# Kernel tuning notes

Measured on AMD Instinct MI355X. Metric: run time of the kernel, lower is better.

Reference implementation:

```python
import jax, jax.numpy as jnp
import numpy as np

D = 3  # input dim, hardcoded in source


def _jet_linear(c0, c1, c2, W, b):
    # Taylor-mode (raw-derivative coefficients) through y = x @ W^T + b.
    # Bias only affects the 0th coefficient; higher coefficients are linear.
    y0 = jnp.einsum('bdi,oi->bdo', c0, W) + b
    y1 = jnp.einsum('bdi,oi->bdo', c1, W)
    y2 = jnp.einsum('bdi,oi->bdo', c2, W)
    return y0, y1, y2


def _jet_tanh(c0, c1, c2):
    # g(t) with g(0)=c0, g'(0)=c1, g''(0)=c2; f = tanh(g):
    #   f(0)  = tanh(c0)
    #   f'(0) = sech^2(c0) * c1
    #   f''(0)= sech^2(c0) * c2 - 2 tanh(c0) sech^2(c0) * c1^2
    y0 = jnp.tanh(c0)
    s = 1.0 - y0 * y0  # sech^2
    y1 = s * c1
    y2 = s * c2 - 2.0 * y0 * s * (c1 * c1)
    return y0, y1, y2


def setup_inputs() -> dict:
    key = jax.random.key(0)
    ks = jax.random.split(key, 7)
    B = 131072
    x = jax.random.normal(ks[0], (B, D), dtype=jnp.float32)
    # Kaiming-ish small init so tanh does not saturate
    W1 = jax.random.normal(ks[1], (128, D), dtype=jnp.float32) * (1.0 / np.sqrt(D))
    b1 = jax.random.normal(ks[2], (128,), dtype=jnp.float32) * 0.01
    W2 = jax.random.normal(ks[3], (64, 128), dtype=jnp.float32) * (1.0 / np.sqrt(128))
    b2 = jax.random.normal(ks[4], (64,), dtype=jnp.float32) * 0.01
    W3 = jax.random.normal(ks[5], (1, 64), dtype=jnp.float32) * (1.0 / np.sqrt(64))
    b3 = jax.random.normal(ks[6], (1,), dtype=jnp.float32) * 0.01
    return {'x': x, 'W1': W1, 'b1': b1, 'W2': W2, 'b2': b2, 'W3': W3, 'b3': b3}


def reference(x, W1, b1, W2, b2, W3, b3):
    # x: [B, D]. Propagate a k=2 jet along each of the D coordinate
    # directions (vmapped over the direction axis d), then sum the 2nd
    # coefficients -> Laplacian. Returns [B, 1].
    B = x.shape[0]
    dt = x.dtype
    X0 = jnp.broadcast_to(x[:, None, :], (B, D, D))            # replicate(x, D)
    X1 = jnp.broadcast_to(jnp.eye(D, dtype=dt), (B, D, D))     # eye(D)
    X2 = jnp.zeros((B, D, D), dtype=dt)                         # zeros(D, D)
    c = _jet_linear(X0, X1, X2, W1, b1)
    c = _jet_tanh(*c)
    c = _jet_linear(*c, W2, b2)
    c = _jet_tanh(*c)
    F0, F1, F2 = _jet_linear(*c, W3, b3)                        # F2: [B, D, 1]
    return F2.sum(axis=1)                                       # sum_vmapped -> [B, 1]
```

## Files before the change

### kernel.cpp

```cpp
#include <hip/hip_runtime.h>


typedef _Float16 h2 __attribute__((ext_vector_type(2)));
typedef _Float16 h4 __attribute__((ext_vector_type(4)));
typedef _Float16 h8 __attribute__((ext_vector_type(8)));
typedef float f32x4 __attribute__((ext_vector_type(4)));

#define BLOCK 256
constexpr int DH1 = 128;
constexpr int DH2 = 64;
constexpr int TILES = 2;

__device__ __forceinline__ float fast_tanh(float x) {
    float e = __builtin_amdgcn_exp2f(x * 2.885390081777926814f);
    return fmaf(-2.0f, __builtin_amdgcn_rcpf(e + 1.0f), 1.0f);
}

__device__ __forceinline__ h2 pk(float a, float b) {
    auto r = __builtin_amdgcn_cvt_pkrtz(a, b);
    return __builtin_bit_cast(h2, r);
}

__device__ __forceinline__ h8 cat4(h2 a, h2 b, h2 c, h2 d) {
    h4 lo = __builtin_shufflevector(a, b, 0, 1, 2, 3);
    h4 hi = __builtin_shufflevector(c, d, 0, 1, 2, 3);
    return __builtin_shufflevector(lo, hi, 0, 1, 2, 3, 4, 5, 6, 7);
}

__global__ __launch_bounds__(BLOCK) void lap_fused(
        const float* __restrict__ x,
        const float* __restrict__ W1, const float* __restrict__ b1,
        const float* __restrict__ W2, const float* __restrict__ b2,
        const float* __restrict__ W3,
        float* __restrict__ out, int B, int ntiles)
{
    __shared__ float4 s_w1p[DH1];
    __shared__ float  s_wq2[DH1];
    __shared__ __align__(16) _Float16 s_a[16][64][8];
    __shared__ __align__(16) float s_b2[DH2];
    __shared__ __align__(16) float s_w3[DH2];

    const int t = threadIdx.x;

    #pragma unroll
    for (int u = 0; u < 4; ++u) {
        const int f   = u * 256 + t;
        const int l   = f & 63;
        const int row = f >> 6;
        const int m   = row & 3;
        const int kk  = row >> 2;
        const int k   = m * 16 + (l & 15);
        const int jr  = kk * 32 + (l >> 4) * 8;
        const float4 wlo = *reinterpret_cast<const float4*>(W2 + k * DH1 + jr);
        const float4 whi = *reinterpret_cast<const float4*>(W2 + k * DH1 + jr + 4);
        *reinterpret_cast<h8*>(&s_a[row][l][0]) =
            cat4(pk(wlo.x, wlo.y), pk(wlo.z, wlo.w),
                 pk(whi.x, whi.y), pk(whi.z, whi.w));
    }
    if (t < DH1) {
        const float wx = W1[t*3+0], wy = W1[t*3+1], wz = W1[t*3+2];
        s_w1p[t] = make_float4(wx, wy, wz, b1[t]);
        s_wq2[t] = -2.0f * (wx*wx + wy*wy + wz*wz);
    }
    if (t < DH2) { s_b2[t] = b2[t]; s_w3[t] = W3[t]; }
    __syncthreads();

    const int lane = t & 63;
    const int wave = t >> 6;
    const int bcol = lane & 15;
    const int g    = lane >> 4;

    #pragma unroll 1
    for (int tile = 0; tile < TILES; ++tile) {
        const int tid = blockIdx.x + tile * gridDim.x;
        if (tid >= ntiles) break;
        const int braw = tid * 64 + wave * 16 + bcol;
        const int b    = (braw < B) ? braw : (B - 1);

        const float x0 = x[b*3+0];
        const float x1 = x[b*3+1];
        const float x2 = x[b*3+2];

        f32x4 acc[5][4];
        #pragma unroll
        for (int f = 0; f < 5; ++f)
            #pragma unroll
            for (int m = 0; m < 4; ++m)
                acc[f][m] = (f32x4){0.f, 0.f, 0.f, 0.f};

        #pragma unroll
        for (int kk = 0; kk < 4; ++kk) {
            h2 P0[4], P1[4], P2[4], P3[4], P4[4];
            #pragma unroll
            for (int ii = 0; ii < 4; ++ii) {
                const int j0 = kk*32 + g*8 + ii*2;
                const float4 wa = s_w1p[j0];
                const float4 wb = s_w1p[j0 + 1];
                const float  qa = s_wq2[j0];
                const float  qb = s_wq2[j0 + 1];

                const float prea = fmaf(x0, wa.x, fmaf(x1, wa.y, fmaf(x2, wa.z, wa.w)));
                const float ea   = __builtin_amdgcn_exp2f(prea * 2.885390081777926814f);
                const float ra   = __builtin_amdgcn_rcpf(ea + 1.0f);
                const float ha   = fmaf(-2.0f, ra, 1.0f);
                const float sa   = fmaf(-ha, ha, 1.0f);

                const float preb = fmaf(x0, wb.x, fmaf(x1, wb.y, fmaf(x2, wb.z, wb.w)));
                const float eb   = __builtin_amdgcn_exp2f(preb * 2.885390081777926814f);
                const float rb   = __builtin_amdgcn_rcpf(eb + 1.0f);
                const float hb   = fmaf(-2.0f, rb, 1.0f);
                const float sb   = fmaf(-hb, hb, 1.0f);

                P0[ii] = pk(ha,          hb);
                P1[ii] = pk(sa * wa.x,   sb * wb.x);
                P2[ii] = pk(sa * wa.y,   sb * wb.y);
                P3[ii] = pk(sa * wa.z,   sb * wb.z);
                P4[ii] = pk((ha*sa)*qa,  (hb*sb)*qb);
            }
            const h8 F0 = cat4(P0[0], P0[1], P0[2], P0[3]);
            const h8 F1 = cat4(P1[0], P1[1], P1[2], P1[3]);
            const h8 F2 = cat4(P2[0], P2[1], P2[2], P2[3]);
            const h8 F3 = cat4(P3[0], P3[1], P3[2], P3[3]);
            const h8 F4 = cat4(P4[0], P4[1], P4[2], P4[3]);

            #pragma unroll
            for (int m = 0; m < 4; ++m) {
                const h8 fa = *reinterpret_cast<const h8*>(&s_a[kk*4 + m][lane][0]);
                acc[0][m] = __builtin_amdgcn_mfma_f32_16x16x32_f16(fa, F0, acc[0][m], 0, 0, 0);
                acc[1][m] = __builtin_amdgcn_mfma_f32_16x16x32_f16(fa, F1, acc[1][m], 0, 0, 0);
                acc[2][m] = __builtin_amdgcn_mfma_f32_16x16x32_f16(fa, F2, acc[2][m], 0, 0, 0);
                acc[3][m] = __builtin_amdgcn_mfma_f32_16x16x32_f16(fa, F3, acc[3][m], 0, 0, 0);
                acc[4][m] = __builtin_amdgcn_mfma_f32_16x16x32_f16(fa, F4, acc[4][m], 0, 0, 0);
            }
        }

        float partial = 0.0f;
        #pragma unroll
        for (int m = 0; m < 4; ++m) {
            const int kb = m*16 + g*4;
            const f32x4 b2v = *reinterpret_cast<const f32x4*>(&s_b2[kb]);
            const f32x4 w3v = *reinterpret_cast<const f32x4*>(&s_w3[kb]);
            #pragma unroll
            for (int r = 0; r < 4; ++r) {
                const float z0 = acc[0][m][r] + b2v[r];
                const float g0 = fast_tanh(z0);
                const float s2 = fmaf(-g0, g0, 1.0f);
                const float qd = acc[1][m][r]*acc[1][m][r]
                               + acc[2][m][r]*acc[2][m][r]
                               + acc[3][m][r]*acc[3][m][r];
                const float G2 = s2 * fmaf(-2.0f * g0, qd, acc[4][m][r]);
                partial = fmaf(w3v[r], G2, partial);
            }
        }

        partial += __shfl_xor(partial, 16);
        partial += __shfl_xor(partial, 32);

        if (g == 0 && braw < B) out[braw] = partial;
    }
}

extern "C" void kernel_launch(void* const* d_in, const int* in_sizes, int n_in,
                              void* d_out, int out_size, void* d_ws, size_t ws_size,
                              hipStream_t stream) {
    const float* x  = (const float*)d_in[0];
    const float* W1 = (const float*)d_in[1];
    const float* b1 = (const float*)d_in[2];
    const float* W2 = (const float*)d_in[3];
    const float* b2 = (const float*)d_in[4];
    const float* W3 = (const float*)d_in[5];
    float* out = (float*)d_out;

    const int B      = in_sizes[0] / 3;
    const int ntiles = (B + 63) / 64;
    const int grid   = (ntiles + TILES - 1) / TILES;
    lap_fused<<<grid, BLOCK, 0, stream>>>(x, W1, b1, W2, b2, W3, out, B, ntiles);
}
```

Before: 25.95 us.

## Double block size, prefetch x for both tiles, fold tanh scale into weights

Blocks grow to 512 threads covering 128 batch rows per tile, which halves the grid and spreads the per-block W2 fp16 staging over twice as many rows. The x values for both tiles are loaded before the shared-memory setup, so their global latency overlaps the weight staging. The 2/ln2 tanh scale is folded into b1, b2 and x, which removes a multiply per activation. The grid drops to 512 blocks, so occupancy and load balance across CUs shift, and the larger blocks need more registers.

```diff
diff --git a/kernel.cpp b/kernel.cpp
--- a/kernel.cpp
+++ b/kernel.cpp
@@ -6,15 +6,11 @@
 typedef _Float16 h8 __attribute__((ext_vector_type(8)));
 typedef float f32x4 __attribute__((ext_vector_type(4)));
 
-#define BLOCK 256
+#define BLOCK 512
 constexpr int DH1 = 128;
 constexpr int DH2 = 64;
 constexpr int TILES = 2;
-
-__device__ __forceinline__ float fast_tanh(float x) {
-    float e = __builtin_amdgcn_exp2f(x * 2.885390081777926814f);
-    return fmaf(-2.0f, __builtin_amdgcn_rcpf(e + 1.0f), 1.0f);
-}
+constexpr float CTANH = 2.885390081777926814f;
 
 __device__ __forceinline__ h2 pk(float a, float b) {
     auto r = __builtin_amdgcn_cvt_pkrtz(a, b);
@@ -37,14 +33,29 @@
     __shared__ float4 s_w1p[DH1];
     __shared__ float  s_wq2[DH1];
     __shared__ __align__(16) _Float16 s_a[16][64][8];
-    __shared__ __align__(16) float s_b2[DH2];
+    __shared__ __align__(16) float s_b2c[DH2];
     __shared__ __align__(16) float s_w3[DH2];
 
-    const int t = threadIdx.x;
+    const int t    = threadIdx.x;
+    const int lane = t & 63;
+    const int wave = t >> 6;
+    const int bcol = lane & 15;
+    const int g    = lane >> 4;
+
+    float xv[TILES][3];
+    #pragma unroll
+    for (int tile = 0; tile < TILES; ++tile) {
+        const int tid  = blockIdx.x + tile * gridDim.x;
+        const int braw = tid * 128 + wave * 16 + bcol;
+        const int b    = (braw < B) ? braw : (B - 1);
+        xv[tile][0] = x[b*3+0];
+        xv[tile][1] = x[b*3+1];
+        xv[tile][2] = x[b*3+2];
+    }
 
     #pragma unroll
-    for (int u = 0; u < 4; ++u) {
-        const int f   = u * 256 + t;
+    for (int u = 0; u < 2; ++u) {
+        const int f   = u * 512 + t;
         const int l   = f & 63;
         const int row = f >> 6;
         const int m   = row & 3;
@@ -59,27 +70,21 @@
     }
     if (t < DH1) {
         const float wx = W1[t*3+0], wy = W1[t*3+1], wz = W1[t*3+2];
-        s_w1p[t] = make_float4(wx, wy, wz, b1[t]);
+        s_w1p[t] = make_float4(wx, wy, wz, CTANH * b1[t]);
         s_wq2[t] = -2.0f * (wx*wx + wy*wy + wz*wz);
     }
-    if (t < DH2) { s_b2[t] = b2[t]; s_w3[t] = W3[t]; }
+    if (t < DH2) { s_b2c[t] = CTANH * b2[t]; s_w3[t] = W3[t]; }
     __syncthreads();
-
-    const int lane = t & 63;
-    const int wave = t >> 6;
-    const int bcol = lane & 15;
-    const int g    = lane >> 4;
 
     #pragma unroll 1
     for (int tile = 0; tile < TILES; ++tile) {
         const int tid = blockIdx.x + tile * gridDim.x;
         if (tid >= ntiles) break;
-        const int braw = tid * 64 + wave * 16 + bcol;
-        const int b    = (braw < B) ? braw : (B - 1);
+        const int braw = tid * 128 + wave * 16 + bcol;
 
-        const float x0 = x[b*3+0];
-        const float x1 = x[b*3+1];
-        const float x2 = x[b*3+2];
+        const float x0c = xv[tile][0] * CTANH;
+        const float x1c = xv[tile][1] * CTANH;
+        const float x2c = xv[tile][2] * CTANH;
 
         f32x4 acc[5][4];
         #pragma unroll
@@ -99,14 +104,14 @@
                 const float  qa = s_wq2[j0];
                 const float  qb = s_wq2[j0 + 1];
 
-                const float prea = fmaf(x0, wa.x, fmaf(x1, wa.y, fmaf(x2, wa.z, wa.w)));
-                const float ea   = __builtin_amdgcn_exp2f(prea * 2.885390081777926814f);
+                const float prea = fmaf(x0c, wa.x, fmaf(x1c, wa.y, fmaf(x2c, wa.z, wa.w)));
+                const float ea   = __builtin_amdgcn_exp2f(prea);
                 const float ra   = __builtin_amdgcn_rcpf(ea + 1.0f);
                 const float ha   = fmaf(-2.0f, ra, 1.0f);
                 const float sa   = fmaf(-ha, ha, 1.0f);
 
-                const float preb = fmaf(x0, wb.x, fmaf(x1, wb.y, fmaf(x2, wb.z, wb.w)));
-                const float eb   = __builtin_amdgcn_exp2f(preb * 2.885390081777926814f);
+                const float preb = fmaf(x0c, wb.x, fmaf(x1c, wb.y, fmaf(x2c, wb.z, wb.w)));
+                const float eb   = __builtin_amdgcn_exp2f(preb);
                 const float rb   = __builtin_amdgcn_rcpf(eb + 1.0f);
                 const float hb   = fmaf(-2.0f, rb, 1.0f);
                 const float sb   = fmaf(-hb, hb, 1.0f);
@@ -138,12 +143,12 @@
         #pragma unroll
         for (int m = 0; m < 4; ++m) {
             const int kb = m*16 + g*4;
-            const f32x4 b2v = *reinterpret_cast<const f32x4*>(&s_b2[kb]);
+            const f32x4 b2v = *reinterpret_cast<const f32x4*>(&s_b2c[kb]);
             const f32x4 w3v = *reinterpret_cast<const f32x4*>(&s_w3[kb]);
             #pragma unroll
             for (int r = 0; r < 4; ++r) {
-                const float z0 = acc[0][m][r] + b2v[r];
-                const float g0 = fast_tanh(z0);
+                const float e0 = __builtin_amdgcn_exp2f(fmaf(CTANH, acc[0][m][r], b2v[r]));
+                const float g0 = fmaf(-2.0f, __builtin_amdgcn_rcpf(e0 + 1.0f), 1.0f);
                 const float s2 = fmaf(-g0, g0, 1.0f);
                 const float qd = acc[1][m][r]*acc[1][m][r]
                                + acc[2][m][r]*acc[2][m][r]
@@ -172,7 +177,7 @@
     float* out = (float*)d_out;
 
     const int B      = in_sizes[0] / 3;
-    const int ntiles = (B + 63) / 64;
+    const int ntiles = (B + 127) / 128;
     const int grid   = (ntiles + TILES - 1) / TILES;
     lap_fused<<<grid, BLOCK, 0, stream>>>(x, W1, b1, W2, b2, W3, out, B, ntiles);
 }
```

Result: slower. 36.63 us (+41.2%).
